# Kernel tuning notes

Measured on AMD Instinct MI355X. Metric: run time of the kernel, lower is better.

Reference implementation:

```python
import jax, jax.numpy as jnp
import numpy as np

D = 1024      # d_model
H = 16        # num_heads
DK = D // H   # head dim
L = 6         # num_layers
DFF = 4 * D   # feed-forward width
V = 32000     # vocab
B = 8         # batch
TP1 = 513     # target tokens (x length); decoded length = 512
S = 1024      # encoder frames
MAXLEN = 512
EPS = 1e-6


def make_pe(max_len, d):
    pos = np.arange(max_len, dtype=np.float64)[:, None]
    i = np.arange(0, d, 2, dtype=np.float64)[None, :]
    ang = pos / np.power(10000.0, i / d)
    pe = np.zeros((max_len, d), dtype=np.float32)
    pe[:, 0::2] = np.sin(ang)
    pe[:, 1::2] = np.cos(ang)
    return jnp.asarray(pe)


def setup_inputs() -> dict:
    key = jax.random.key(0)
    ks = jax.random.split(key, 16)
    sc = 0.02
    inp = {
        'x': jax.random.randint(ks[0], (B, TP1), 0, V, dtype=jnp.int64),
        'encoder_output': jax.random.normal(ks[1], (B, S, D), jnp.float32),
        'emb': jax.random.normal(ks[2], (V, D), jnp.float32) * sc,
        'pe': make_pe(MAXLEN, D),
        # per-layer stacked params; index 0..3 = q,k,v,out projections (in,out layout)
        'attn1_w': jax.random.normal(ks[3], (L, 4, D, D), jnp.float32) * sc,
        'attn1_b': jnp.zeros((L, 4, D), jnp.float32),
        'attn2_w': jax.random.normal(ks[4], (L, 4, D, D), jnp.float32) * sc,
        'attn2_b': jnp.zeros((L, 4, D), jnp.float32),
        'norm_a': jnp.ones((L, 3, D), jnp.float32),
        'norm_b': jnp.zeros((L, 3, D), jnp.float32),
        'ff1_w': jax.random.normal(ks[5], (L, D, DFF), jnp.float32) * sc,
        'ff1_b': jnp.zeros((L, DFF), jnp.float32),
        'ff2_w': jax.random.normal(ks[6], (L, DFF, D), jnp.float32) * sc,
        'ff2_b': jnp.zeros((L, D), jnp.float32),
        'fc_w': jax.random.normal(ks[7], (D, V), jnp.float32) * sc,
        'fc_b': jnp.zeros((V,), jnp.float32),
    }
    return inp


def _norm(x, a, b):
    mu = jnp.mean(x, axis=-1, keepdims=True)
    # torch .std() default is unbiased (ddof=1)
    var = jnp.sum((x - mu) ** 2, axis=-1, keepdims=True) / (x.shape[-1] - 1)
    return a * (x - mu) / (jnp.sqrt(var) + EPS) + b


def _mha(q_in, kv_in, w, b):
    # w: [4, D, D], b: [4, D]; masks in the original are no-ops (bug), omitted.
    bs, tq, _ = q_in.shape
    q = (q_in @ w[0] + b[0]).reshape(bs, tq, H, DK).transpose(0, 2, 1, 3)
    k = (kv_in @ w[1] + b[1]).reshape(bs, -1, H, DK).transpose(0, 2, 1, 3)
    v = (kv_in @ w[2] + b[2]).reshape(bs, -1, H, DK).transpose(0, 2, 1, 3)
    score = jnp.einsum('bhqd,bhkd->bhqk', q, k) / np.sqrt(DK).astype(np.float32)
    attn = jax.nn.softmax(score, axis=-1)
    o = jnp.einsum('bhqk,bhkd->bhqd', attn, v)
    o = o.transpose(0, 2, 1, 3).reshape(bs, tq, D)
    return o @ w[3] + b[3]


def reference(x, encoder_output, emb, pe, attn1_w, attn1_b, attn2_w, attn2_b,
              norm_a, norm_b, ff1_w, ff1_b, ff2_w, ff2_b, fc_w, fc_b):
    t = x.shape[1] - 1
    h = emb[x[:, :-1]] + pe[None, :t, :]  # [B, T, D]
    for l in range(L):
        a1 = _mha(h, h, attn1_w[l], attn1_b[l])
        h = _norm(a1 + h, norm_a[l, 0], norm_b[l, 0])
        a2 = _mha(h, encoder_output, attn2_w[l], attn2_b[l])
        h = _norm(a2 + h, norm_a[l, 1], norm_b[l, 1])
        f = jax.nn.relu(h @ ff1_w[l] + ff1_b[l]) @ ff2_w[l] + ff2_b[l]
        h = _norm(f + h, norm_a[l, 2], norm_b[l, 2])
    logits = h @ fc_w + fc_b  # [B, T, V]
    return jax.nn.log_softmax(logits, axis=-1)
```

## Files before the change

kernel.cpp:

```cpp
#include <hip/hip_runtime.h>

typedef __attribute__((ext_vector_type(4))) float f32x4;
typedef __attribute__((ext_vector_type(8))) __bf16 bfx8;
typedef unsigned short u16;
typedef unsigned int u32;

__device__ __forceinline__ u16 f2bf(float f) {
  u32 u = __builtin_bit_cast(u32, f);
  u = (u + 0x7FFFu + ((u >> 16) & 1u)) >> 16;
  return (u16)u;
}
__device__ __forceinline__ float bf2f(u16 u) {
  return __builtin_bit_cast(float, ((u32)u) << 16);
}

typedef __attribute__((address_space(1))) const void gvoid;
typedef __attribute__((address_space(3))) void svoid;
__device__ __forceinline__ void gload16(const void* g, void* l) {
  __builtin_amdgcn_global_load_lds((gvoid*)g, (svoid*)l, 16, 0, 0);
}

__device__ __forceinline__ float wredsum(float v) {
#pragma unroll
  for (int o = 32; o; o >>= 1) v += __shfl_xor(v, o, 64);
  return v;
}
__device__ __forceinline__ float wredmax(float v) {
#pragma unroll
  for (int o = 32; o; o >>= 1) v = fmaxf(v, __shfl_xor(v, o, 64));
  return v;
}

__global__ __launch_bounds__(256) void wconv_kernel(const float* __restrict__ in,
                                                    u16* __restrict__ out, int K, int N) {
  __shared__ u16 tile[32][33];
  const long z = blockIdx.z;
  const float* iz = in + z * (long)K * N;
  u16* oz = out + z * (long)K * N;
  const int n0 = blockIdx.x << 5, k0 = blockIdx.y << 5;
  const int tx = threadIdx.x & 31, ty = threadIdx.x >> 5;
#pragma unroll
  for (int i = 0; i < 4; ++i)
    tile[ty + 8 * i][tx] = f2bf(iz[(long)(k0 + ty + 8 * i) * N + n0 + tx]);
  __syncthreads();
#pragma unroll
  for (int i = 0; i < 4; ++i)
    oz[(long)(n0 + ty + 8 * i) * K + k0 + tx] = tile[tx][ty + 8 * i];
}

__global__ __launch_bounds__(256) void cvt_kernel(const float* __restrict__ in,
                                                  u16* __restrict__ out, long n) {
  long i = ((long)blockIdx.x * 256 + threadIdx.x) * 4;
  if (i + 3 < n) {
    float4 v = *(const float4*)(in + i);
    ushort4 o = {f2bf(v.x), f2bf(v.y), f2bf(v.z), f2bf(v.w)};
    *(ushort4*)(out + i) = o;
  }
}

__global__ __launch_bounds__(256) void embed_kernel(const int* __restrict__ x,
                                                    const float* __restrict__ emb,
                                                    const float* __restrict__ pe,
                                                    float* __restrict__ h,
                                                    u16* __restrict__ hb) {
  const int row = blockIdx.x;
  const int b = row >> 9, t = row & 511;
  const long tok = (long)x[b * 513 + t];
  const int d = threadIdx.x << 2;
  float4 e = *(const float4*)(emb + tok * 1024 + d);
  float4 p = *(const float4*)(pe + (long)t * 1024 + d);
  float4 v = {e.x + p.x, e.y + p.y, e.z + p.z, e.w + p.w};
  *(float4*)(h + (long)row * 1024 + d) = v;
  ushort4 o = {f2bf(v.x), f2bf(v.y), f2bf(v.z), f2bf(v.w)};
  *(ushort4*)(hb + (long)row * 1024 + d) = o;
}

template <int NP>
__global__ __launch_bounds__(256) void addnorm_kernel(const u16* __restrict__ pb,
                                                      float* __restrict__ h,
                                                      u16* __restrict__ hb,
                                                      const float* __restrict__ ga,
                                                      const float* __restrict__ gb) {
  __shared__ float r1[4], r2[4];
  const long row = blockIdx.x;
  const int d = threadIdx.x << 2;
  float4 a = *(const float4*)(h + row * 1024 + d);
  float x0 = a.x, x1 = a.y, x2 = a.z, x3 = a.w;
#pragma unroll
  for (int n = 0; n < NP; ++n) {
    ushort4 q = *(const ushort4*)(pb + (long)n * 4194304 + row * 1024 + d);
    x0 += bf2f(q.x); x1 += bf2f(q.y); x2 += bf2f(q.z); x3 += bf2f(q.w);
  }
  float s1 = wredsum(x0 + x1 + x2 + x3);
  float s2 = wredsum(x0 * x0 + x1 * x1 + x2 * x2 + x3 * x3);
  if ((threadIdx.x & 63) == 0) { r1[threadIdx.x >> 6] = s1; r2[threadIdx.x >> 6] = s2; }
  __syncthreads();
  float S1 = r1[0] + r1[1] + r1[2] + r1[3];
  float S2 = r2[0] + r2[1] + r2[2] + r2[3];
  float mu = S1 * (1.0f / 1024.0f);
  float var = (S2 - S1 * mu) * (1.0f / 1023.0f);
  float inv = 1.0f / (sqrtf(fmaxf(var, 0.f)) + 1e-6f);
  float4 g4 = *(const float4*)(ga + d);
  float4 b4 = *(const float4*)(gb + d);
  float y0 = g4.x * (x0 - mu) * inv + b4.x;
  float y1 = g4.y * (x1 - mu) * inv + b4.y;
  float y2 = g4.z * (x2 - mu) * inv + b4.z;
  float y3 = g4.w * (x3 - mu) * inv + b4.w;
  float4 y = {y0, y1, y2, y3};
  *(float4*)(h + row * 1024 + d) = y;
  ushort4 o = {f2bf(y0), f2bf(y1), f2bf(y2), f2bf(y3)};
  *(ushort4*)(hb + row * 1024 + d) = o;
}

__global__ __launch_bounds__(256) void logsoftmax_kernel(float* __restrict__ lg) {
  const long row = blockIdx.x;
  float* lr = lg + row * 32000L;
  float m = -1e30f, s = 0.f;
  for (int j = threadIdx.x; j < 8000; j += 256) {
    float4 v = *(const float4*)(lr + (long)j * 4);
    float lm = fmaxf(fmaxf(v.x, v.y), fmaxf(v.z, v.w));
    if (lm > m) { s *= __expf(m - lm); m = lm; }
    s += __expf(v.x - m) + __expf(v.y - m) + __expf(v.z - m) + __expf(v.w - m);
  }
#pragma unroll
  for (int o = 32; o; o >>= 1) {
    float om = __shfl_xor(m, o, 64), os = __shfl_xor(s, o, 64);
    float M = fmaxf(m, om);
    s = s * __expf(m - M) + os * __expf(om - M);
    m = M;
  }
  __shared__ float rm[4], rs[4];
  if ((threadIdx.x & 63) == 0) { rm[threadIdx.x >> 6] = m; rs[threadIdx.x >> 6] = s; }
  __syncthreads();
  float M = fmaxf(fmaxf(rm[0], rm[1]), fmaxf(rm[2], rm[3]));
  float S = rs[0] * __expf(rm[0] - M) + rs[1] * __expf(rm[1] - M) +
            rs[2] * __expf(rm[2] - M) + rs[3] * __expf(rm[3] - M);
  float lse = M + __logf(S);
  for (int j = threadIdx.x; j < 8000; j += 256) {
    float4 v = *(const float4*)(lr + (long)j * 4);
    v.x -= lse; v.y -= lse; v.z -= lse; v.w -= lse;
    *(float4*)(lr + (long)j * 4) = v;
  }
}

__global__ __launch_bounds__(512) void logsoftmax_bf16_kernel(const u16* __restrict__ lg,
                                                              float* __restrict__ out) {
  __shared__ u16 rl[32000];
  __shared__ float rr[8];
  const long row = blockIdx.x;
  const u16* lr = lg + row * 32000L;
  float* od = out + row * 32000L;
  const int tid = threadIdx.x;
  float m0 = -1e30f, m1 = -1e30f;
  for (int j = tid * 8; j < 32000; j += 4096) {
    ushort4 a = *(const ushort4*)(lr + j);
    ushort4 b = *(const ushort4*)(lr + j + 4);
    *(ushort4*)&rl[j] = a;
    *(ushort4*)&rl[j + 4] = b;
    m0 = fmaxf(m0, fmaxf(fmaxf(bf2f(a.x), bf2f(a.y)), fmaxf(bf2f(a.z), bf2f(a.w))));
    m1 = fmaxf(m1, fmaxf(fmaxf(bf2f(b.x), bf2f(b.y)), fmaxf(bf2f(b.z), bf2f(b.w))));
  }
  float m = wredmax(fmaxf(m0, m1));
  if ((tid & 63) == 0) rr[tid >> 6] = m;
  __syncthreads();
  m = fmaxf(fmaxf(fmaxf(rr[0], rr[1]), fmaxf(rr[2], rr[3])),
            fmaxf(fmaxf(rr[4], rr[5]), fmaxf(rr[6], rr[7])));
  __syncthreads();
  float s0 = 0.f, s1 = 0.f;
  for (int j = tid * 8; j < 32000; j += 4096) {
    ushort4 a = *(const ushort4*)&rl[j];
    ushort4 b = *(const ushort4*)&rl[j + 4];
    s0 += __expf(bf2f(a.x) - m) + __expf(bf2f(a.y) - m) +
          __expf(bf2f(a.z) - m) + __expf(bf2f(a.w) - m);
    s1 += __expf(bf2f(b.x) - m) + __expf(bf2f(b.y) - m) +
          __expf(bf2f(b.z) - m) + __expf(bf2f(b.w) - m);
  }
  float s = wredsum(s0 + s1);
  if ((tid & 63) == 0) rr[tid >> 6] = s;
  __syncthreads();
  s = rr[0] + rr[1] + rr[2] + rr[3] + rr[4] + rr[5] + rr[6] + rr[7];
  const float lse = m + __logf(s);
  for (int j = tid * 8; j < 32000; j += 4096) {
    ushort4 a = *(const ushort4*)&rl[j];
    ushort4 b = *(const ushort4*)&rl[j + 4];
    float4 o0 = {bf2f(a.x) - lse, bf2f(a.y) - lse, bf2f(a.z) - lse, bf2f(a.w) - lse};
    float4 o1 = {bf2f(b.x) - lse, bf2f(b.y) - lse, bf2f(b.z) - lse, bf2f(b.w) - lse};
    *(float4*)(od + j) = o0;
    *(float4*)(od + j + 4) = o1;
  }
}

template <int SKV>
__global__ __launch_bounds__(512) void attn_kernel(const u16* __restrict__ Q,
                                                   const u16* __restrict__ Kb,
                                                   const u16* __restrict__ Vt,
                                                   u16* __restrict__ ctx) {
  __shared__ u16 Kl[2][4096];
  __shared__ u16 Vl[2][4096];
  __shared__ u16 Pl[8][16][72];
  const int tid = threadIdx.x, lane = tid & 63, wave = tid >> 6;
  const int l15 = lane & 15, lg = lane >> 4;
  const int bh = blockIdx.y;
  const int qrow = blockIdx.x * 128 + wave * 16 + l15;
  const u16* qp = Q + ((long)bh * 512 + qrow) * 64 + lg * 8;
  bfx8 qf0 = *(const bfx8*)(qp);
  bfx8 qf1 = *(const bfx8*)(qp + 32);

  const int srow = tid >> 3;
  const int schunk = (tid & 7) ^ (srow & 7);
  const u16* Kbb = Kb + ((long)bh * SKV + srow) * 64 + schunk * 8;
  const u16* Vtb2 = Vt + ((long)bh * 64 + srow) * SKV + schunk * 8;

  auto stage = [&](int t, int buf) {
    const int kv0 = t * 64;
    gload16(Kbb + (long)kv0 * 64, &Kl[buf][tid * 8]);
    gload16(Vtb2 + kv0, &Vl[buf][tid * 8]);
  };

  const f32x4 zf = {0.f, 0.f, 0.f, 0.f};
  f32x4 acc_o[4] = {zf, zf, zf, zf};
  float mrun = -1e30f, lrun = 0.f;
  const int swk = l15 & 7;
  constexpr int NT = SKV / 64;

  stage(0, 0);
  __syncthreads();
  int buf = 0;
#pragma unroll 1
  for (int t = 0; t < NT; ++t) {
    if (t + 1 < NT) stage(t + 1, buf ^ 1);
    f32x4 sacc[4];
    __builtin_amdgcn_s_setprio(1);
#pragma unroll
    for (int kvt = 0; kvt < 4; ++kvt) {
      const int krow = kvt * 16 + l15;
      bfx8 kf0 = *(const bfx8*)&Kl[buf][krow * 64 + ((lg ^ swk) << 3)];
      bfx8 kf1 = *(const bfx8*)&Kl[buf][krow * 64 + (((4 + lg) ^ swk) << 3)];
      f32x4 tt = __builtin_amdgcn_mfma_f32_16x16x32_bf16(kf0, qf0, zf, 0, 0, 0);
      sacc[kvt] = __builtin_amdgcn_mfma_f32_16x16x32_bf16(kf1, qf1, tt, 0, 0, 0);
    }
    __builtin_amdgcn_s_setprio(0);
    float pm = -1e30f;
#pragma unroll
    for (int kvt = 0; kvt < 4; ++kvt)
#pragma unroll
      for (int r = 0; r < 4; ++r) pm = fmaxf(pm, sacc[kvt][r]);
    pm = fmaxf(pm, __shfl_xor(pm, 16, 64));
    pm = fmaxf(pm, __shfl_xor(pm, 32, 64));
    pm *= 0.125f;
    const bool grow = !__all(pm <= mrun);
    const float mnew = grow ? fmaxf(mrun, pm) : mrun;
    float psum = 0.f;
#pragma unroll
    for (int kvt = 0; kvt < 4; ++kvt)
#pragma unroll
      for (int r = 0; r < 4; ++r) {
        float p = __expf(sacc[kvt][r] * 0.125f - mnew);
        psum += p;
        Pl[wave][l15][kvt * 16 + lg * 4 + r] = f2bf(p);
      }
    psum += __shfl_xor(psum, 16, 64);
    psum += __shfl_xor(psum, 32, 64);
    if (grow) {
      const float corr = __expf(mrun - mnew);
      lrun = lrun * corr + psum;
      mrun = mnew;
#pragma unroll
      for (int dt = 0; dt < 4; ++dt) {
        acc_o[dt][0] *= corr; acc_o[dt][1] *= corr;
        acc_o[dt][2] *= corr; acc_o[dt][3] *= corr;
      }
    } else {
      lrun += psum;
    }
    bfx8 pf0 = *(const bfx8*)&Pl[wave][l15][lg * 8];
    bfx8 pf1 = *(const bfx8*)&Pl[wave][l15][32 + lg * 8];
    __builtin_amdgcn_s_setprio(1);
#pragma unroll
    for (int dt = 0; dt < 4; ++dt) {
      const int vrow = dt * 16 + l15;
      bfx8 vf0 = *(const bfx8*)&Vl[buf][vrow * 64 + ((lg ^ swk) << 3)];
      bfx8 vf1 = *(const bfx8*)&Vl[buf][vrow * 64 + (((4 + lg) ^ swk) << 3)];
      acc_o[dt] = __builtin_amdgcn_mfma_f32_16x16x32_bf16(vf0, pf0, acc_o[dt], 0, 0, 0);
      acc_o[dt] = __builtin_amdgcn_mfma_f32_16x16x32_bf16(vf1, pf1, acc_o[dt], 0, 0, 0);
    }
    __builtin_amdgcn_s_setprio(0);
    __syncthreads();
    buf ^= 1;
  }
  const float inv = 1.0f / lrun;
  const int b = bh >> 4, hh = bh & 15;
  u16* crow = ctx + ((long)b * 512 + qrow) * 1024 + hh * 64;
#pragma unroll
  for (int dt = 0; dt < 4; ++dt)
#pragma unroll
    for (int r = 0; r < 4; ++r)
      crow[dt * 16 + lg * 4 + r] = f2bf(acc_o[dt][r] * inv);
}

template <int BM, int BN, int WMW, int WNW, int EPI, bool RELU>
__global__ __launch_bounds__(256) void gemm_bt(const u16* __restrict__ A, long sAz, int lda,
                                               const u16* __restrict__ Bt, long sBz, int ldb,
                                               const float* __restrict__ bias,
                                               void* __restrict__ out, long sCz, int ldc,
                                               int K, int Ttok) {
  constexpr int WROWS = BM / WMW, WCOLS = BN / WNW;
  constexpr int MI = WROWS / 16, NI = WCOLS / 16;
  __shared__ u16 As[BM * 32];
  __shared__ u16 Bs[BN * 32];
  const int tid = threadIdx.x, lane = tid & 63, wave = tid >> 6;
  const int l15 = lane & 15, lg = lane >> 4;
  const int wm = wave / WNW, wn = wave % WNW;
  const int bx = blockIdx.x, by = blockIdx.y;
  const long z = blockIdx.z;
  const int srow = tid >> 2, scol = (tid & 3) << 3;
  const u16* Aa = A + z * sAz + (long)(by * BM + srow) * lda + scol;
  const u16* Ba = Bt + z * sBz + (long)(bx * BN + srow) * ldb + scol;

  f32x4 acc[MI][NI];
#pragma unroll
  for (int i = 0; i < MI; ++i)
#pragma unroll
    for (int j = 0; j < NI; ++j) acc[i][j] = (f32x4){0.f, 0.f, 0.f, 0.f};

  for (int kt = 0; kt < K; kt += 32) {
#pragma unroll
    for (int i = 0; i < BM / 64; ++i)
      gload16(Aa + (long)i * 64 * lda + kt, &As[i * 2048 + tid * 8]);
#pragma unroll
    for (int i = 0; i < BN / 64; ++i)
      gload16(Ba + (long)i * 64 * ldb + kt, &Bs[i * 2048 + tid * 8]);
    __syncthreads();
    bfx8 afr[MI], bfr[NI];
#pragma unroll
    for (int i = 0; i < MI; ++i)
      afr[i] = *(const bfx8*)&As[(wm * WROWS + i * 16 + l15) * 32 + (lg << 3)];
#pragma unroll
    for (int j = 0; j < NI; ++j)
      bfr[j] = *(const bfx8*)&Bs[(wn * WCOLS + j * 16 + l15) * 32 + (lg << 3)];
#pragma unroll
    for (int i = 0; i < MI; ++i)
#pragma unroll
      for (int j = 0; j < NI; ++j)
        acc[i][j] = __builtin_amdgcn_mfma_f32_16x16x32_bf16(afr[i], bfr[j], acc[i][j], 0, 0, 0);
    __syncthreads();
  }

  const int gm0 = by * BM + wm * WROWS;
  const int gn0 = bx * BN + wn * WCOLS;
#pragma unroll
  for (int i = 0; i < MI; ++i) {
#pragma unroll
    for (int j = 0; j < NI; ++j) {
      const int gn = gn0 + j * 16 + l15;
      const float bv = (bias && z == 0) ? bias[gn] : 0.f;
#pragma unroll
      for (int r = 0; r < 4; ++r) {
        const int gm = gm0 + i * 16 + (lg << 2) + r;
        float v = acc[i][j][r] + bv;
        if (RELU) v = fmaxf(v, 0.f);
        if constexpr (EPI == 0) {
          ((float*)out)[z * sCz + (long)gm * ldc + gn] = v;
        } else if constexpr (EPI == 1) {
          ((u16*)out)[z * sCz + (long)gm * ldc + gn] = f2bf(v);
        } else if constexpr (EPI == 3) {
          const int b = gm / Ttok, t = gm - b * Ttok;
          const int hh = gn >> 6, dk = gn & 63;
          ((u16*)out)[(((long)(b * 16 + hh) * Ttok + t) << 6) + dk] = f2bf(v);
        }
      }
    }
  }
}

#define MMAQ(hm, hn)                                                                   \
  {                                                                                    \
    _Pragma("unroll") for (int kk = 0; kk < 2; ++kk)                                   \
        _Pragma("unroll") for (int i = 0; i < 4; ++i)                                  \
            _Pragma("unroll") for (int jn = 0; jn < 2; ++jn)                           \
                acc[(hm)*4 + i][(hn)*2 + jn] = __builtin_amdgcn_mfma_f32_16x16x32_bf16( \
                    a[i][kk], b[jn][kk], acc[(hm)*4 + i][(hn)*2 + jn], 0, 0, 0);       \
  }

template <int EPI, bool RELU, int BMAP>
__global__ __launch_bounds__(512, 2) void gemm256(const u16* __restrict__ A, int lda,
                                                  const u16* __restrict__ Bt, int ldb,
                                                  const float* __restrict__ bias,
                                                  void* __restrict__ out, int ldc, int K,
                                                  int Ttok, void* __restrict__ out2,
                                                  void* __restrict__ out3, int gx) {
  __shared__ u16 lds[2][2][2][8192];
  const int tid = threadIdx.x, lane = tid & 63;
  const int wid = tid >> 6, wm = wid >> 2, wn = wid & 3;
  const int l15 = lane & 15, lg = lane >> 4;
  const int S = gx >> 3;
  const int xcd = blockIdx.x & 7, idx = blockIdx.x >> 3;
  const int mt = xcd * S + idx % S;
  const int nt_ = idx / S;
  const int NT = K >> 6;

  const int r0 = tid >> 3;
  const int blkx = (tid & 7) ^ (r0 & 7);
  const int n0 = nt_ * 256;
  long brow0;
  if constexpr (BMAP == 1)
    brow0 = (long)(n0 >> 11) * 4096 + 1024 + (n0 & 2047);
  else
    brow0 = n0;
  const u16* Abase = A + (long)(mt * 256 + r0) * lda + blkx * 8;
  const u16* Bbase = Bt + (brow0 + r0) * ldb + blkx * 8;

  auto stageA = [&](int s, int half) {
    const int kts = (s < NT ? s : NT - 1) << 6;
    const u16* g = Abase + (long)(half * 128) * lda + kts;
    gload16(g, &lds[s & 1][0][half][tid * 8]);
    gload16(g + (long)64 * lda, &lds[s & 1][0][half][(512 + tid) * 8]);
  };
  auto stageB = [&](int s, int half) {
    const int kts = (s < NT ? s : NT - 1) << 6;
    const u16* g = Bbase + (long)(half * 128) * ldb + kts;
    gload16(g, &lds[s & 1][1][half][tid * 8]);
    gload16(g + (long)64 * ldb, &lds[s & 1][1][half][(512 + tid) * 8]);
  };

  f32x4 acc[8][4];
#pragma unroll
  for (int i = 0; i < 8; ++i)
#pragma unroll
    for (int j = 0; j < 4; ++j) acc[i][j] = (f32x4){0.f, 0.f, 0.f, 0.f};
  bfx8 a[4][2], b[2][2];

  const int sw = l15 & 7;
  auto loadA = [&](int buf, int hm) {
#pragma unroll
    for (int i = 0; i < 4; ++i) {
      const int row = hm * 64 + i * 16 + l15;
#pragma unroll
      for (int kk = 0; kk < 2; ++kk)
        a[i][kk] = *(const bfx8*)&lds[buf][0][wm][row * 64 + (((kk * 4 + lg) ^ sw) << 3)];
    }
  };
  auto loadB = [&](int buf, int hn) {
#pragma unroll
    for (int jn = 0; jn < 2; ++jn) {
      const int row = (wn & 1) * 64 + hn * 32 + jn * 16 + l15;
#pragma unroll
      for (int kk = 0; kk < 2; ++kk)
        b[jn][kk] = *(const bfx8*)&lds[buf][1][wn >> 1][row * 64 + (((kk * 4 + lg) ^ sw) << 3)];
    }
  };

  stageA(0, 0); stageA(0, 1); stageB(0, 0); stageB(0, 1);
  stageA(1, 0); stageA(1, 1);
  asm volatile("s_waitcnt vmcnt(4)" ::: "memory");
  __builtin_amdgcn_s_barrier();

  for (int t = 0; t < NT; ++t) {
    const int p = t & 1;
    loadA(p, 0); loadB(p, 0);
    stageB(t + 1, 0);
    __builtin_amdgcn_s_barrier();
    asm volatile("s_waitcnt lgkmcnt(0)" ::: "memory");
    __builtin_amdgcn_s_setprio(1);
    MMAQ(0, 0);
    __builtin_amdgcn_s_setprio(0);
    __builtin_amdgcn_s_barrier();
    loadB(p, 1);
    stageB(t + 1, 1);
    __builtin_amdgcn_s_barrier();
    asm volatile("s_waitcnt lgkmcnt(0)" ::: "memory");
    __builtin_amdgcn_s_setprio(1);
    MMAQ(0, 1);
    __builtin_amdgcn_s_setprio(0);
    __builtin_amdgcn_s_barrier();
    loadA(p, 1); loadB(p, 0);
    stageA(t + 2, 0);
    __builtin_amdgcn_s_barrier();
    asm volatile("s_waitcnt lgkmcnt(0)" ::: "memory");
    __builtin_amdgcn_s_setprio(1);
    MMAQ(1, 0);
    __builtin_amdgcn_s_setprio(0);
    __builtin_amdgcn_s_barrier();
    loadB(p, 1);
    stageA(t + 2, 1);
    asm volatile("s_waitcnt vmcnt(4)" ::: "memory");
    __builtin_amdgcn_s_barrier();
    asm volatile("s_waitcnt lgkmcnt(0)" ::: "memory");
    __builtin_amdgcn_s_setprio(1);
    MMAQ(1, 1);
    __builtin_amdgcn_s_setprio(0);
    __builtin_amdgcn_s_barrier();
  }

  const int gm0 = mt * 256 + wm * 128;
  const int gn0 = nt_ * 256 + wn * 64;
#pragma unroll
  for (int ii = 0; ii < 8; ++ii) {
#pragma unroll
    for (int jj = 0; jj < 4; ++jj) {
      const int gn = gn0 + jj * 16 + l15;
      float bv;
      if constexpr (BMAP == 1)
        bv = bias[(gn >> 11) * 4096 + 1024 + (gn & 2047)];
      else
        bv = bias ? bias[gn] : 0.f;
#pragma unroll
      for (int r = 0; r < 4; ++r) {
        const int gm = gm0 + ii * 16 + (lg << 2) + r;
        float v = acc[ii][jj][r] + bv;
        if (RELU) v = fmaxf(v, 0.f);
        if constexpr (EPI == 0) {
          ((float*)out)[(long)gm * ldc + gn] = v;
        } else if constexpr (EPI == 1) {
          ((u16*)out)[(long)gm * ldc + gn] = f2bf(v);
        } else if constexpr (EPI == 6) {
          const int bq = gm / Ttok, t2 = gm - bq * Ttok;
          const int sec = gn >> 10, w1 = gn & 1023;
          const int hh = w1 >> 6, dk = w1 & 63;
          const u16 val = f2bf(v);
          if (sec == 0)
            ((u16*)out)[(((long)(bq * 16 + hh) * Ttok + t2) << 6) + dk] = val;
          else if (sec == 1)
            ((u16*)out2)[(((long)(bq * 16 + hh) * Ttok + t2) << 6) + dk] = val;
          else
            ((u16*)out3)[((long)((bq * 16 + hh) << 6) + dk) * Ttok + t2] = val;
        } else if constexpr (EPI == 7) {
          const int bq = gm / Ttok, t2 = gm - bq * Ttok;
          const int sec = gn >> 10, w1 = gn & 1023;
          const int hh = w1 >> 6, dk = w1 & 63;
          const u16 val = f2bf(v);
          if (sec == 0)
            ((u16*)out)[(((long)(bq * 16 + hh) * Ttok + t2) << 6) + dk] = val;
          else
            ((u16*)out2)[((long)((bq * 16 + hh) << 6) + dk) * Ttok + t2] = val;
        } else if constexpr (EPI == 8) {
          const int l = gn >> 11, inner = gn & 2047;
          const int sec = inner >> 10, w1 = inner & 1023;
          const int hh = w1 >> 6, dk = w1 & 63;
          const int bq = gm >> 10, t2 = gm & 1023;
          const u16 val = f2bf(v);
          if (sec == 0)
            ((u16*)out)[((((long)l * 8 + bq) * 16 + hh) * 1024 + t2) * 64 + dk] = val;
          else
            ((u16*)out2)[((((long)l * 8 + bq) * 16 + hh) * 64 + dk) * 1024 + t2] = val;
        }
      }
    }
  }
}

extern "C" void kernel_launch(void* const* d_in, const int* in_sizes, int n_in,
                              void* d_out, int out_size, void* d_ws, size_t ws_size,
                              hipStream_t stream) {
  const int* x = (const int*)d_in[0];
  const float* enc = (const float*)d_in[1];
  const float* emb = (const float*)d_in[2];
  const float* pe = (const float*)d_in[3];
  const float* a1w = (const float*)d_in[4];
  const float* a1b = (const float*)d_in[5];
  const float* a2w = (const float*)d_in[6];
  const float* a2b = (const float*)d_in[7];
  const float* nra = (const float*)d_in[8];
  const float* nrb = (const float*)d_in[9];
  const float* f1w = (const float*)d_in[10];
  const float* f1b = (const float*)d_in[11];
  const float* f2w = (const float*)d_in[12];
  const float* f2b = (const float*)d_in[13];
  const float* fcw = (const float*)d_in[14];
  const float* fcb = (const float*)d_in[15];
  float* out = (float*)d_out;

  char* base = (char*)d_ws;
  size_t off = 0;
  auto alloc = [&](size_t bytes) -> void* {
    void* p = base + off;
    off += (bytes + 255) & ~(size_t)255;
    return p;
  };
  const long wsz = 1024 * 1024;
  const bool big = ws_size >= (600ull << 20);
  u16* wT = (u16*)alloc(96ull * wsz * 2);
  u16* encb = (u16*)alloc(8ull * wsz * 2);
  float* h = (float*)alloc(4ull * wsz * 4);
  u16* hb = (u16*)alloc(4ull * wsz * 2);
  u16* qb = (u16*)alloc(4ull * wsz * 2);
  u16* kb = (u16*)alloc(8ull * wsz * 2);
  u16* vtb = (u16*)alloc(8ull * wsz * 2);
  u16* ctxb = (u16*)alloc(4ull * wsz * 2);
  u16* pb = (u16*)alloc(16ull * wsz * 2);
  u16* midb = (u16*)alloc(16ull * wsz * 2);
  u16* fcT = qb;
  u16* kv6 = big ? (u16*)alloc(262144000) : nullptr;
  u16* kb6 = kv6;
  u16* vtb6 = kv6 ? kv6 + 50331648 : nullptr;
  u16* lgb = kv6;

  u16* wTa1 = wT;
  u16* wTa2 = wT + 24 * wsz;
  u16* wTf1 = wT + 48 * wsz;
  u16* wTf2 = wT + 72 * wsz;

  cvt_kernel<<<dim3(8192), dim3(256), 0, stream>>>(enc, encb, 8ll * wsz);
  embed_kernel<<<dim3(4096), dim3(256), 0, stream>>>(x, emb, pe, h, hb);
  wconv_kernel<<<dim3(32, 32, 24), dim3(256), 0, stream>>>(a1w, wTa1, 1024, 1024);
  wconv_kernel<<<dim3(32, 32, 24), dim3(256), 0, stream>>>(a2w, wTa2, 1024, 1024);
  wconv_kernel<<<dim3(128, 32, 6), dim3(256), 0, stream>>>(f1w, wTf1, 1024, 4096);
  wconv_kernel<<<dim3(32, 128, 6), dim3(256), 0, stream>>>(f2w, wTf2, 4096, 1024);

  if (big) {
    gemm256<8, false, 1><<<dim3(1536), dim3(512), 0, stream>>>(
        encb, 1024, wTa2, 1024, a2b, kb6, 0, 1024, 1024, vtb6, nullptr, 32);
  }

  for (int l = 0; l < 6; ++l) {
    const float* b1 = a1b + (long)l * 4096;
    const float* b2 = a2b + (long)l * 4096;
    const u16* w1 = wTa1 + (long)l * 4 * wsz;
    const u16* w2 = wTa2 + (long)l * 4 * wsz;

    gemm256<6, false, 0><<<dim3(192), dim3(512), 0, stream>>>(
        hb, 1024, w1, 1024, b1, qb, 0, 1024, 512, kb, vtb, 16);
    attn_kernel<512><<<dim3(4, 128), dim3(512), 0, stream>>>(qb, kb, vtb, ctxb);
    gemm_bt<128, 128, 2, 2, 1, false><<<dim3(8, 32, 2), dim3(256), 0, stream>>>(
        ctxb, 512, 1024, w1 + 3 * wsz, 512, 1024, b1 + 3072, pb, 4194304, 1024, 512, 0);
    addnorm_kernel<2><<<dim3(4096), dim3(256), 0, stream>>>(
        pb, h, hb, nra + (l * 3 + 0) * 1024, nrb + (l * 3 + 0) * 1024);

    gemm_bt<64, 128, 2, 2, 3, false><<<dim3(8, 64, 1), dim3(256), 0, stream>>>(
        hb, 0, 1024, w2, 0, 1024, b2, qb, 0, 0, 1024, 512);
    const u16* lK;
    const u16* lV;
    if (big) {
      lK = kb6 + (long)l * 8388608;
      lV = vtb6 + (long)l * 8388608;
    } else {
      gemm256<7, false, 0><<<dim3(256), dim3(512), 0, stream>>>(
          encb, 1024, w2 + wsz, 1024, b2 + 1024, kb, 0, 1024, 1024, vtb, nullptr, 32);
      lK = kb;
      lV = vtb;
    }
    attn_kernel<1024><<<dim3(4, 128), dim3(512), 0, stream>>>(qb, lK, lV, ctxb);
    gemm_bt<128, 128, 2, 2, 1, false><<<dim3(8, 32, 2), dim3(256), 0, stream>>>(
        ctxb, 512, 1024, w2 + 3 * wsz, 512, 1024, b2 + 3072, pb, 4194304, 1024, 512, 0);
    addnorm_kernel<2><<<dim3(4096), dim3(256), 0, stream>>>(
        pb, h, hb, nra + (l * 3 + 1) * 1024, nrb + (l * 3 + 1) * 1024);

    gemm256<1, true, 0><<<dim3(256), dim3(512), 0, stream>>>(
        hb, 1024, wTf1 + (long)l * 4 * wsz, 1024, f1b + (long)l * 4096, midb, 4096, 1024, 0,
        nullptr, nullptr, 16);
    gemm_bt<128, 128, 2, 2, 1, false><<<dim3(8, 32, 4), dim3(256), 0, stream>>>(
        midb, 1024, 4096, wTf2 + (long)l * 4 * wsz, 1024, 4096, f2b + (long)l * 1024, pb,
        4194304, 1024, 1024, 0);
    addnorm_kernel<4><<<dim3(4096), dim3(256), 0, stream>>>(
        pb, h, hb, nra + (l * 3 + 2) * 1024, nrb + (l * 3 + 2) * 1024);
  }

  wconv_kernel<<<dim3(1000, 32, 1), dim3(256), 0, stream>>>(fcw, fcT, 1024, 32000);
  if (big) {
    gemm256<1, false, 0><<<dim3(2000), dim3(512), 0, stream>>>(
        hb, 1024, fcT, 1024, fcb, lgb, 32000, 1024, 0, nullptr, nullptr, 16);
    logsoftmax_bf16_kernel<<<dim3(4096), dim3(512), 0, stream>>>(lgb, out);
  } else {
    gemm256<0, false, 0><<<dim3(2000), dim3(512), 0, stream>>>(
        hb, 1024, fcT, 1024, fcb, out, 32000, 1024, 0, nullptr, nullptr, 16);
    logsoftmax_kernel<<<dim3(4096), dim3(256), 0, stream>>>(out);
  }
}
```

Before: 3.035 ms.

## Widen weight transpose tiles and add N-chunked XCD block mapping for big GEMMs

```diff
diff --git a/kernel.cpp b/kernel.cpp
--- a/kernel.cpp
+++ b/kernel.cpp
@@ -33,19 +33,29 @@
 
 __global__ __launch_bounds__(256) void wconv_kernel(const float* __restrict__ in,
                                                     u16* __restrict__ out, int K, int N) {
-  __shared__ u16 tile[32][33];
+  __shared__ u16 tile[64][69];
   const long z = blockIdx.z;
   const float* iz = in + z * (long)K * N;
   u16* oz = out + z * (long)K * N;
-  const int n0 = blockIdx.x << 5, k0 = blockIdx.y << 5;
-  const int tx = threadIdx.x & 31, ty = threadIdx.x >> 5;
-#pragma unroll
-  for (int i = 0; i < 4; ++i)
-    tile[ty + 8 * i][tx] = f2bf(iz[(long)(k0 + ty + 8 * i) * N + n0 + tx]);
+  const int n0 = blockIdx.x << 6, k0 = blockIdx.y << 6;
+  const int tr = threadIdx.x >> 4;
+  const int tc4 = (threadIdx.x & 15) << 2;
+#pragma unroll
+  for (int i = 0; i < 4; ++i) {
+    const int r = tr + i * 16;
+    float4 v = *(const float4*)(iz + (long)(k0 + r) * N + n0 + tc4);
+    tile[r][tc4] = f2bf(v.x);
+    tile[r][tc4 + 1] = f2bf(v.y);
+    tile[r][tc4 + 2] = f2bf(v.z);
+    tile[r][tc4 + 3] = f2bf(v.w);
+  }
   __syncthreads();
 #pragma unroll
-  for (int i = 0; i < 4; ++i)
-    oz[(long)(n0 + ty + 8 * i) * K + k0 + tx] = tile[tx][ty + 8 * i];
+  for (int i = 0; i < 4; ++i) {
+    const int n = tr + i * 16;
+    ushort4 o = {tile[tc4][n], tile[tc4 + 1][n], tile[tc4 + 2][n], tile[tc4 + 3][n]};
+    *(ushort4*)(oz + (long)(n0 + n) * K + k0 + tc4) = o;
+  }
 }
 
 __global__ __launch_bounds__(256) void cvt_kernel(const float* __restrict__ in,
@@ -382,7 +392,7 @@
                     a[i][kk], b[jn][kk], acc[(hm)*4 + i][(hn)*2 + jn], 0, 0, 0);       \
   }
 
-template <int EPI, bool RELU, int BMAP>
+template <int EPI, bool RELU, int BMAP, bool NCH>
 __global__ __launch_bounds__(512, 2) void gemm256(const u16* __restrict__ A, int lda,
                                                   const u16* __restrict__ Bt, int ldb,
                                                   const float* __restrict__ bias,
@@ -393,10 +403,16 @@
   const int tid = threadIdx.x, lane = tid & 63;
   const int wid = tid >> 6, wm = wid >> 2, wn = wid & 3;
   const int l15 = lane & 15, lg = lane >> 4;
-  const int S = gx >> 3;
   const int xcd = blockIdx.x & 7, idx = blockIdx.x >> 3;
-  const int mt = xcd * S + idx % S;
-  const int nt_ = idx / S;
+  int mt, nt_;
+  if constexpr (NCH) {
+    mt = idx % gx;
+    nt_ = xcd * ((gridDim.x >> 3) / gx) + idx / gx;
+  } else {
+    const int S = gx >> 3;
+    mt = xcd * S + idx % S;
+    nt_ = idx / S;
+  }
   const int NT = K >> 6;
 
   const int r0 = tid >> 3;
@@ -499,6 +515,9 @@
 #pragma unroll
     for (int jj = 0; jj < 4; ++jj) {
       const int gn = gn0 + jj * 16 + l15;
+      if constexpr (EPI <= 1) {
+        if (Ttok && gn >= Ttok) continue;
+      }
       float bv;
       if constexpr (BMAP == 1)
         bv = bias[(gn >> 11) * 4096 + 1024 + (gn & 2047)];
@@ -602,13 +621,13 @@
 
   cvt_kernel<<<dim3(8192), dim3(256), 0, stream>>>(enc, encb, 8ll * wsz);
   embed_kernel<<<dim3(4096), dim3(256), 0, stream>>>(x, emb, pe, h, hb);
-  wconv_kernel<<<dim3(32, 32, 24), dim3(256), 0, stream>>>(a1w, wTa1, 1024, 1024);
-  wconv_kernel<<<dim3(32, 32, 24), dim3(256), 0, stream>>>(a2w, wTa2, 1024, 1024);
-  wconv_kernel<<<dim3(128, 32, 6), dim3(256), 0, stream>>>(f1w, wTf1, 1024, 4096);
-  wconv_kernel<<<dim3(32, 128, 6), dim3(256), 0, stream>>>(f2w, wTf2, 4096, 1024);
+  wconv_kernel<<<dim3(16, 16, 24), dim3(256), 0, stream>>>(a1w, wTa1, 1024, 1024);
+  wconv_kernel<<<dim3(16, 16, 24), dim3(256), 0, stream>>>(a2w, wTa2, 1024, 1024);
+  wconv_kernel<<<dim3(64, 16, 6), dim3(256), 0, stream>>>(f1w, wTf1, 1024, 4096);
+  wconv_kernel<<<dim3(16, 64, 6), dim3(256), 0, stream>>>(f2w, wTf2, 4096, 1024);
 
   if (big) {
-    gemm256<8, false, 1><<<dim3(1536), dim3(512), 0, stream>>>(
+    gemm256<8, false, 1, true><<<dim3(1536), dim3(512), 0, stream>>>(
         encb, 1024, wTa2, 1024, a2b, kb6, 0, 1024, 1024, vtb6, nullptr, 32);
   }
 
@@ -618,7 +637,7 @@
     const u16* w1 = wTa1 + (long)l * 4 * wsz;
     const u16* w2 = wTa2 + (long)l * 4 * wsz;
 
-    gemm256<6, false, 0><<<dim3(192), dim3(512), 0, stream>>>(
+    gemm256<6, false, 0, false><<<dim3(192), dim3(512), 0, stream>>>(
         hb, 1024, w1, 1024, b1, qb, 0, 1024, 512, kb, vtb, 16);
     attn_kernel<512><<<dim3(4, 128), dim3(512), 0, stream>>>(qb, kb, vtb, ctxb);
     gemm_bt<128, 128, 2, 2, 1, false><<<dim3(8, 32, 2), dim3(256), 0, stream>>>(
@@ -634,7 +653,7 @@
       lK = kb6 + (long)l * 8388608;
       lV = vtb6 + (long)l * 8388608;
     } else {
-      gemm256<7, false, 0><<<dim3(256), dim3(512), 0, stream>>>(
+      gemm256<7, false, 0, false><<<dim3(256), dim3(512), 0, stream>>>(
           encb, 1024, w2 + wsz, 1024, b2 + 1024, kb, 0, 1024, 1024, vtb, nullptr, 32);
       lK = kb;
       lV = vtb;
@@ -645,7 +664,7 @@
     addnorm_kernel<2><<<dim3(4096), dim3(256), 0, stream>>>(
         pb, h, hb, nra + (l * 3 + 1) * 1024, nrb + (l * 3 + 1) * 1024);
 
-    gemm256<1, true, 0><<<dim3(256), dim3(512), 0, stream>>>(
+    gemm256<1, true, 0, false><<<dim3(256), dim3(512), 0, stream>>>(
         hb, 1024, wTf1 + (long)l * 4 * wsz, 1024, f1b + (long)l * 4096, midb, 4096, 1024, 0,
         nullptr, nullptr, 16);
     gemm_bt<128, 128, 2, 2, 1, false><<<dim3(8, 32, 4), dim3(256), 0, stream>>>(
@@ -655,14 +674,14 @@
         pb, h, hb, nra + (l * 3 + 2) * 1024, nrb + (l * 3 + 2) * 1024);
   }
 
-  wconv_kernel<<<dim3(1000, 32, 1), dim3(256), 0, stream>>>(fcw, fcT, 1024, 32000);
+  wconv_kernel<<<dim3(500, 16, 1), dim3(256), 0, stream>>>(fcw, fcT, 1024, 32000);
   if (big) {
-    gemm256<1, false, 0><<<dim3(2000), dim3(512), 0, stream>>>(
-        hb, 1024, fcT, 1024, fcb, lgb, 32000, 1024, 0, nullptr, nullptr, 16);
+    gemm256<1, false, 0, true><<<dim3(2048), dim3(512), 0, stream>>>(
+        hb, 1024, fcT, 1024, fcb, lgb, 32000, 1024, 32000, nullptr, nullptr, 16);
     logsoftmax_bf16_kernel<<<dim3(4096), dim3(512), 0, stream>>>(lgb, out);
   } else {
-    gemm256<0, false, 0><<<dim3(2000), dim3(512), 0, stream>>>(
-        hb, 1024, fcT, 1024, fcb, out, 32000, 1024, 0, nullptr, nullptr, 16);
+    gemm256<0, false, 0, true><<<dim3(2048), dim3(512), 0, stream>>>(
+        hb, 1024, fcT, 1024, fcb, out, 32000, 1024, 32000, nullptr, nullptr, 16);
     logsoftmax_kernel<<<dim3(4096), dim3(256), 0, stream>>>(out);
   }
 }
```

Measured after the change: 3.059 ms. Within noise of the previous version (+0.8%).
